# Performance work log

Measured on AMD Instinct MI355X. Metric: run time of the kernel, lower is better.

## Reference

```python
import jax, jax.numpy as jnp
import numpy as np

B, L, D, H = 2, 2048, 1024, 16
P = D // H  # head dim = 64


def setup_inputs() -> dict:
    key = jax.random.key(0)
    ks = jax.random.split(key, 9)
    s = 1.0 / np.sqrt(D)
    x = jax.random.normal(ks[0], (B, L, D), dtype=jnp.float32)
    Wq = jax.random.normal(ks[1], (D, D), dtype=jnp.float32) * s
    bq = jax.random.normal(ks[2], (D,), dtype=jnp.float32) * 0.02
    Wk = jax.random.normal(ks[3], (D, D), dtype=jnp.float32) * s
    bk = jax.random.normal(ks[4], (D,), dtype=jnp.float32) * 0.02
    Wv = jax.random.normal(ks[5], (D, D), dtype=jnp.float32) * s
    bv = jax.random.normal(ks[6], (D,), dtype=jnp.float32) * 0.02
    Wo = jax.random.normal(ks[7], (D, D), dtype=jnp.float32) * s
    bo = jax.random.normal(ks[8], (D,), dtype=jnp.float32) * 0.02
    return {"token_activations": x, "Wq": Wq, "bq": bq, "Wk": Wk, "bk": bk,
            "Wv": Wv, "bv": bv, "Wo": Wo, "bo": bo}


def _split_heads(t):
    # 'b l (h p) -> b h l p'
    b, l, d = t.shape
    return t.reshape(b, l, H, P).transpose(0, 2, 1, 3)


def reference(token_activations, Wq, bq, Wk, bk, Wv, bv, Wo, bo):
    x = token_activations
    q = _split_heads(x @ Wq.T + bq)  # [B,H,L,P]
    k = _split_heads(x @ Wk.T + bk)
    v = _split_heads(x @ Wv.T + bv)
    # pattern[b,h,l,m] = K_l . Q_m / sqrt(P)
    scores = jnp.einsum('bhlp,bhmp->bhlm', k, q) / jnp.sqrt(jnp.float32(P))
    attn = jax.nn.softmax(scores, axis=-2)  # softmax over key axis l
    # out at query position m: sum_l attn[l,m] * V_l
    o = jnp.einsum('bhlm,bhlp->bhmp', attn, v)  # [B,H,L,P] (m indexed)
    o = o.transpose(0, 2, 1, 3).reshape(x.shape[0], x.shape[1], D)  # 'b h m p -> b m (h p)'
    return o @ Wo.T + bo
```

## Files before the change

kernel.cpp:

```cpp
#include <hip/hip_runtime.h>

typedef unsigned short u16;
typedef float f32x4 __attribute__((ext_vector_type(4)));
typedef __bf16 bf16x8 __attribute__((ext_vector_type(8)));
typedef __bf16 bf16x4 __attribute__((ext_vector_type(4)));

#define DEV static __device__ __forceinline__

constexpr int kB = 2;
constexpr int kL = 2048;
constexpr int kD = 1024;
constexpr int kH = 16;
constexpr int kP = 64;
constexpr int kM = kB * kL;
constexpr float kQScale = 0.125f * 1.44269504088896f;

DEV u16 f2bf(float x) {
  union { float f; unsigned u; } v;
  v.f = x;
  unsigned r = v.u + 0x7fffu + ((v.u >> 16) & 1u);
  return (u16)(r >> 16);
}

DEV void gload16(const void* g, void* l) {
  __builtin_amdgcn_global_load_lds(
      (const __attribute__((address_space(1))) unsigned int*)g,
      (__attribute__((address_space(3))) unsigned int*)l, 16, 0, 0);
}

__global__ void cvt_kernel(const float* __restrict__ src, u16* __restrict__ dst, int n4) {
  int i = blockIdx.x * blockDim.x + threadIdx.x;
  if (i >= n4) return;
  float4 v = reinterpret_cast<const float4*>(src)[i];
  uint2 o;
  o.x = (unsigned)f2bf(v.x) | ((unsigned)f2bf(v.y) << 16);
  o.y = (unsigned)f2bf(v.z) | ((unsigned)f2bf(v.w) << 16);
  reinterpret_cast<uint2*>(dst)[i] = o;
}

__global__ void cvtw_kernel(const float* __restrict__ w0, const float* __restrict__ w1,
                            const float* __restrict__ w2, const float* __restrict__ w3,
                            u16* __restrict__ o0, u16* __restrict__ o1,
                            u16* __restrict__ o2, u16* __restrict__ o3) {
  int sel = blockIdx.x >> 10;
  int i = (blockIdx.x & 1023) * 256 + threadIdx.x;
  const float* src = sel == 0 ? w0 : (sel == 1 ? w1 : (sel == 2 ? w2 : w3));
  u16* dst = sel == 0 ? o0 : (sel == 1 ? o1 : (sel == 2 ? o2 : o3));
  float4 v = reinterpret_cast<const float4*>(src)[i];
  uint2 o;
  o.x = (unsigned)f2bf(v.x) | ((unsigned)f2bf(v.y) << 16);
  o.y = (unsigned)f2bf(v.z) | ((unsigned)f2bf(v.w) << 16);
  reinterpret_cast<uint2*>(dst)[i] = o;
}

template <bool SWAP>
DEV void gemm_tile(const u16* __restrict__ A, const u16* __restrict__ W,
                   int m0, int n0, u16* As, u16* Bs, f32x4 acc[4][4]) {
  const int tid = threadIdx.x;
  const int w = tid >> 6, lane = tid & 63;
  const int wr = w >> 1, wc = w & 1;
  const int g = lane >> 4, c = lane & 15;
  const int srow = lane >> 2;
  const int skoff = ((lane & 3) ^ (srow & 3)) * 8;
  const int rsl0 = (g ^ (c & 3)) * 8;

  for (int k0 = 0; k0 < kD; k0 += 32) {
    __syncthreads();
#pragma unroll
    for (int j = 0; j < 2; ++j) {
      const u16* ga = A + (size_t)(m0 + w * 32 + j * 16 + srow) * kD + k0 + skoff;
      gload16(ga, As + (w * 32 + j * 16) * 32);
      const u16* gb = W + (size_t)(n0 + w * 32 + j * 16 + srow) * kD + k0 + skoff;
      gload16(gb, Bs + (w * 32 + j * 16) * 32);
    }
    __syncthreads();

    bf16x8 af[4], bfr[4];
#pragma unroll
    for (int f = 0; f < 4; ++f) {
      af[f]  = *reinterpret_cast<const bf16x8*>(As + (wr * 64 + f * 16 + c) * 32 + rsl0);
      bfr[f] = *reinterpret_cast<const bf16x8*>(Bs + (wc * 64 + f * 16 + c) * 32 + rsl0);
    }
#pragma unroll
    for (int fi = 0; fi < 4; ++fi)
#pragma unroll
      for (int fj = 0; fj < 4; ++fj) {
        if constexpr (SWAP)
          acc[fj][fi] = __builtin_amdgcn_mfma_f32_16x16x32_bf16(bfr[fj], af[fi], acc[fj][fi], 0, 0, 0);
        else
          acc[fi][fj] = __builtin_amdgcn_mfma_f32_16x16x32_bf16(af[fi], bfr[fj], acc[fi][fj], 0, 0, 0);
      }
  }
}

__global__ __launch_bounds__(256) void qkv_kernel(
    const u16* __restrict__ xb,
    const u16* __restrict__ wq, const u16* __restrict__ wk, const u16* __restrict__ wv,
    const float* __restrict__ bq, const float* __restrict__ bk, const float* __restrict__ bv,
    u16* __restrict__ qb, u16* __restrict__ kb, u16* __restrict__ vtb) {
  __shared__ u16 As[128 * 32], Bs[128 * 32];
  const int mb = blockIdx.x, nb = blockIdx.y;
  const int sel = nb >> 3;
  const int m0 = mb * 128, n0 = (nb & 7) * 128;
  const u16* W = sel == 0 ? wq : (sel == 1 ? wk : wv);
  const float* bias = sel == 0 ? bq : (sel == 1 ? bk : bv);

  const int lane = threadIdx.x & 63, w = threadIdx.x >> 6;
  const int wr = w >> 1, wc = w & 1, g = lane >> 4, c = lane & 15;
  const int bb = m0 >> 11;
  const int lbase = (m0 & 2047) + wr * 64;

  f32x4 acc[4][4];
#pragma unroll
  for (int i = 0; i < 4; ++i)
#pragma unroll
    for (int j = 0; j < 4; ++j) acc[i][j] = f32x4{0.f, 0.f, 0.f, 0.f};

  if (sel < 2) {
    gemm_tile<true>(xb, W, m0, n0, As, Bs, acc);
    u16* dst = sel == 0 ? qb : kb;
    const float scale = (sel == 0) ? kQScale : 1.0f;
#pragma unroll
    for (int fj = 0; fj < 4; ++fj) {
      const int n4 = n0 + wc * 64 + fj * 16 + g * 4;
      const float4 b4 = *reinterpret_cast<const float4*>(&bias[n4]);
      const int hh = n4 >> 6, p0 = n4 & 63;
      u16* base = dst + ((size_t)(bb * kH + hh)) * kL * kP + p0;
#pragma unroll
      for (int fi = 0; fi < 4; ++fi) {
        const int l = lbase + fi * 16 + c;
        bf16x4 o;
        o[0] = (__bf16)((acc[fj][fi][0] + b4.x) * scale);
        o[1] = (__bf16)((acc[fj][fi][1] + b4.y) * scale);
        o[2] = (__bf16)((acc[fj][fi][2] + b4.z) * scale);
        o[3] = (__bf16)((acc[fj][fi][3] + b4.w) * scale);
        *reinterpret_cast<bf16x4*>(base + (size_t)l * kP) = o;
      }
    }
  } else {
    gemm_tile<false>(xb, W, m0, n0, As, Bs, acc);
#pragma unroll
    for (int fj = 0; fj < 4; ++fj) {
      const int n = n0 + wc * 64 + fj * 16 + c;
      const float bv_ = bias[n];
      const int hh = n >> 6, p = n & 63;
      u16* base = vtb + (((size_t)(bb * kH + hh)) * kP + p) * kL;
#pragma unroll
      for (int fi = 0; fi < 4; ++fi) {
        const int l4 = lbase + fi * 16 + g * 4;
        bf16x4 o;
#pragma unroll
        for (int r = 0; r < 4; ++r) o[r] = (__bf16)(acc[fi][fj][r] + bv_);
        *reinterpret_cast<bf16x4*>(base + l4) = o;
      }
    }
  }
}

__global__ __launch_bounds__(256) void out_kernel(
    const u16* __restrict__ ob, const u16* __restrict__ wo,
    const float* __restrict__ bo, float* __restrict__ out) {
  __shared__ u16 As[128 * 32], Bs[128 * 32];
  const int m0 = blockIdx.x * 128, n0 = blockIdx.y * 128;
  f32x4 acc[4][4];
#pragma unroll
  for (int i = 0; i < 4; ++i)
#pragma unroll
    for (int j = 0; j < 4; ++j) acc[i][j] = f32x4{0.f, 0.f, 0.f, 0.f};

  gemm_tile<true>(ob, wo, m0, n0, As, Bs, acc);

  const int lane = threadIdx.x & 63, w = threadIdx.x >> 6;
  const int wr = w >> 1, wc = w & 1, g = lane >> 4, c = lane & 15;
#pragma unroll
  for (int fj = 0; fj < 4; ++fj) {
    const int n4 = n0 + wc * 64 + fj * 16 + g * 4;
    const float4 b4 = *reinterpret_cast<const float4*>(&bo[n4]);
#pragma unroll
    for (int fi = 0; fi < 4; ++fi) {
      const int m = m0 + wr * 64 + fi * 16 + c;
      float4 o;
      o.x = acc[fj][fi][0] + b4.x;
      o.y = acc[fj][fi][1] + b4.y;
      o.z = acc[fj][fi][2] + b4.z;
      o.w = acc[fj][fi][3] + b4.w;
      *reinterpret_cast<float4*>(&out[(size_t)m * kD + n4]) = o;
    }
  }
}

__global__ __launch_bounds__(512, 2) void attn_kernel(
    const u16* __restrict__ qb, const u16* __restrict__ kb,
    const u16* __restrict__ vtb, u16* __restrict__ ob) {
  __shared__ __align__(16) char kvs[2][2][8192];
  __shared__ __align__(16) char pts[8][2048];
  const int tid = threadIdx.x, w = tid >> 6, lane = tid & 63;
  const int g = lane >> 4, c = lane & 15;
  const int h = blockIdx.y, b = blockIdx.z;
  const size_t hoff = ((size_t)(b * kH + h)) * kL * kP;
  const char* Qg = (const char*)(qb + hoff);
  const char* Kg = (const char*)(kb + hoff);
  const char* Vg = (const char*)(vtb + hoff);
  const int q0 = blockIdx.x * 128 + w * 16;

  const int lrow = lane >> 3;
  const int spb = ((lane & 7) ^ lrow) << 4;
  const char* kp = Kg + (size_t)(w * 8 + lrow) * 128 + spb;
  const char* vp = Vg + (size_t)(w * 8 + lrow) * (kL * 2) + spb;

  auto stage = [&](int buf) {
    gload16(kp, &kvs[buf][0][w * 1024]);
    gload16(vp, &kvs[buf][1][w * 1024]);
    kp += 64 * 128;
    vp += 128;
  };

  const int csw = (c & 7) << 4;
  const int kvb0 = c * 128 + ((g * 16) ^ csw);
  const int kvb1 = c * 128 + ((64 + g * 16) ^ csw);
  char* myPt = &pts[w][0];

  bf16x8 qf[2];
#pragma unroll
  for (int kc = 0; kc < 2; ++kc)
    qf[kc] = *reinterpret_cast<const bf16x8*>(Qg + (size_t)(q0 + c) * 128 + kc * 64 + g * 16);

  f32x4 oacc[4];
#pragma unroll
  for (int pt = 0; pt < 4; ++pt) oacc[pt] = f32x4{0.f, 0.f, 0.f, 0.f};
  float Srun = 0.f;

  stage(0);
  __syncthreads();

  constexpr int NT = kL / 64;
  auto body = [&](int cur, int t) {
    if (t + 1 < NT) stage(cur ^ 1);
    const char* Ks = &kvs[cur][0][0];
    const char* Vs = &kvs[cur][1][0];

    f32x4 s[4];
    __builtin_amdgcn_s_setprio(1);
#pragma unroll
    for (int lt = 0; lt < 4; ++lt) {
      bf16x8 k0 = *reinterpret_cast<const bf16x8*>(Ks + lt * 2048 + kvb0);
      bf16x8 k1 = *reinterpret_cast<const bf16x8*>(Ks + lt * 2048 + kvb1);
      f32x4 z = f32x4{0.f, 0.f, 0.f, 0.f};
      z = __builtin_amdgcn_mfma_f32_16x16x32_bf16(k0, qf[0], z, 0, 0, 0);
      z = __builtin_amdgcn_mfma_f32_16x16x32_bf16(k1, qf[1], z, 0, 0, 0);
      s[lt] = z;
    }
    __builtin_amdgcn_s_setprio(0);

    float tsum = 0.f;
#pragma unroll
    for (int lt = 0; lt < 4; ++lt) {
      bf16x4 pv;
#pragma unroll
      for (int r = 0; r < 4; ++r) {
        float p = __builtin_amdgcn_exp2f(s[lt][r]);
        tsum += p;
        pv[r] = (__bf16)p;
      }
      *reinterpret_cast<bf16x4*>(myPt + c * 128 + ((lt * 32 + g * 8) ^ csw)) = pv;
    }
    Srun += tsum;

    bf16x8 pf0 = *reinterpret_cast<const bf16x8*>(myPt + kvb0);
    bf16x8 pf1 = *reinterpret_cast<const bf16x8*>(myPt + kvb1);
    __builtin_amdgcn_s_setprio(1);
#pragma unroll
    for (int pt = 0; pt < 4; ++pt) {
      bf16x8 v0 = *reinterpret_cast<const bf16x8*>(Vs + pt * 2048 + kvb0);
      bf16x8 v1 = *reinterpret_cast<const bf16x8*>(Vs + pt * 2048 + kvb1);
      oacc[pt] = __builtin_amdgcn_mfma_f32_16x16x32_bf16(pf0, v0, oacc[pt], 0, 0, 0);
      oacc[pt] = __builtin_amdgcn_mfma_f32_16x16x32_bf16(pf1, v1, oacc[pt], 0, 0, 0);
    }
    __builtin_amdgcn_s_setprio(0);
    __syncthreads();
  };

  for (int t = 0; t < NT; t += 2) {
    body(0, t);
    body(1, t + 1);
  }

  Srun += __shfl_xor(Srun, 16, 64);
  Srun += __shfl_xor(Srun, 32, 64);

  float rs = 1.f / Srun;
  float fr[4];
#pragma unroll
  for (int r = 0; r < 4; ++r) fr[r] = __shfl(rs, g * 4 + r, 64);
#pragma unroll
  for (int pt = 0; pt < 4; ++pt)
#pragma unroll
    for (int r = 0; r < 4; ++r) {
      int q = q0 + g * 4 + r;
      ob[((size_t)(b * kL + q)) * kD + h * kP + pt * 16 + c] = f2bf(oacc[pt][r] * fr[r]);
    }
}

extern "C" void kernel_launch(void* const* d_in, const int* in_sizes, int n_in,
                              void* d_out, int out_size, void* d_ws, size_t ws_size,
                              hipStream_t stream) {
  (void)in_sizes; (void)n_in; (void)out_size; (void)ws_size;
  const float* x  = (const float*)d_in[0];
  const float* Wq = (const float*)d_in[1];
  const float* bq = (const float*)d_in[2];
  const float* Wk = (const float*)d_in[3];
  const float* bk = (const float*)d_in[4];
  const float* Wv = (const float*)d_in[5];
  const float* bv = (const float*)d_in[6];
  const float* Wo = (const float*)d_in[7];
  const float* bo = (const float*)d_in[8];
  float* out = (float*)d_out;

  char* ws = (char*)d_ws;
  u16* xb  = (u16*)(ws);
  u16* wqb = (u16*)(ws + (8u << 20));
  u16* wkb = (u16*)(ws + (10u << 20));
  u16* wvb = (u16*)(ws + (12u << 20));
  u16* wob = (u16*)(ws + (14u << 20));
  u16* qb  = (u16*)(ws + (16u << 20));
  u16* kb  = (u16*)(ws + (24u << 20));
  u16* vtb = (u16*)(ws + (32u << 20));

  cvt_kernel<<<kM * kD / 1024, 256, 0, stream>>>(x, xb, kM * kD / 4);
  cvtw_kernel<<<4096, 256, 0, stream>>>(Wq, Wk, Wv, Wo, wqb, wkb, wvb, wob);

  qkv_kernel<<<dim3(kM / 128, 24), 256, 0, stream>>>(
      xb, wqb, wkb, wvb, bq, bk, bv, qb, kb, vtb);

  attn_kernel<<<dim3(kL / 128, kH, kB), 512, 0, stream>>>(qb, kb, vtb, xb);

  out_kernel<<<dim3(kM / 128, kD / 128), 256, 0, stream>>>(xb, wob, bo, out);
}
```

Before: 117.6 us.

## Merge conversion kernels, remap GEMM blocks across XCDs, widen output GEMM to 512 threads

Combines the activation and weight bf16 conversion kernels into one launch to save a kernel launch. Remaps QKV and output GEMM block indices so that consecutive hardware blocks spread across the 8 XCDs, which is meant to improve L2 locality. Rewrites the output projection to use 8 waves per 128x128 tile with a smaller per-wave accumulator, giving more waves to hide latency. In exchange, each output wave issues more LDS reads per MFMA.

Result: no change. 116.2 us (-1.2%).

```diff
diff --git a/kernel.cpp b/kernel.cpp
--- a/kernel.cpp
+++ b/kernel.cpp
@@ -28,29 +28,29 @@
       (__attribute__((address_space(3))) unsigned int*)l, 16, 0, 0);
 }
 
-__global__ void cvt_kernel(const float* __restrict__ src, u16* __restrict__ dst, int n4) {
+__global__ void cvt_all(const float* __restrict__ x,
+                        const float* __restrict__ w0, const float* __restrict__ w1,
+                        const float* __restrict__ w2, const float* __restrict__ w3,
+                        u16* __restrict__ xb,
+                        u16* __restrict__ o0, u16* __restrict__ o1,
+                        u16* __restrict__ o2, u16* __restrict__ o3) {
   int i = blockIdx.x * blockDim.x + threadIdx.x;
-  if (i >= n4) return;
-  float4 v = reinterpret_cast<const float4*>(src)[i];
+  const float* src;
+  u16* dst;
+  int j;
+  if (i < (1 << 20)) {
+    src = x; dst = xb; j = i;
+  } else {
+    int s = (i >> 18) & 3;
+    j = i & ((1 << 18) - 1);
+    src = s == 0 ? w0 : (s == 1 ? w1 : (s == 2 ? w2 : w3));
+    dst = s == 0 ? o0 : (s == 1 ? o1 : (s == 2 ? o2 : o3));
+  }
+  float4 v = reinterpret_cast<const float4*>(src)[j];
   uint2 o;
   o.x = (unsigned)f2bf(v.x) | ((unsigned)f2bf(v.y) << 16);
   o.y = (unsigned)f2bf(v.z) | ((unsigned)f2bf(v.w) << 16);
-  reinterpret_cast<uint2*>(dst)[i] = o;
-}
-
-__global__ void cvtw_kernel(const float* __restrict__ w0, const float* __restrict__ w1,
-                            const float* __restrict__ w2, const float* __restrict__ w3,
-                            u16* __restrict__ o0, u16* __restrict__ o1,
-                            u16* __restrict__ o2, u16* __restrict__ o3) {
-  int sel = blockIdx.x >> 10;
-  int i = (blockIdx.x & 1023) * 256 + threadIdx.x;
-  const float* src = sel == 0 ? w0 : (sel == 1 ? w1 : (sel == 2 ? w2 : w3));
-  u16* dst = sel == 0 ? o0 : (sel == 1 ? o1 : (sel == 2 ? o2 : o3));
-  float4 v = reinterpret_cast<const float4*>(src)[i];
-  uint2 o;
-  o.x = (unsigned)f2bf(v.x) | ((unsigned)f2bf(v.y) << 16);
-  o.y = (unsigned)f2bf(v.z) | ((unsigned)f2bf(v.w) << 16);
-  reinterpret_cast<uint2*>(dst)[i] = o;
+  reinterpret_cast<uint2*>(dst)[j] = o;
 }
 
 template <bool SWAP>
@@ -99,7 +99,9 @@
     const float* __restrict__ bq, const float* __restrict__ bk, const float* __restrict__ bv,
     u16* __restrict__ qb, u16* __restrict__ kb, u16* __restrict__ vtb) {
   __shared__ u16 As[128 * 32], Bs[128 * 32];
-  const int mb = blockIdx.x, nb = blockIdx.y;
+  const int hw = blockIdx.x;
+  const int logical = (hw & 7) * 96 + (hw >> 3);
+  const int mb = logical & 31, nb = logical >> 5;
   const int sel = nb >> 3;
   const int m0 = mb * 128, n0 = (nb & 7) * 128;
   const u16* W = sel == 0 ? wq : (sel == 1 ? wk : wv);
@@ -157,24 +159,55 @@
   }
 }
 
-__global__ __launch_bounds__(256) void out_kernel(
+__global__ __launch_bounds__(512) void out_kernel(
     const u16* __restrict__ ob, const u16* __restrict__ wo,
     const float* __restrict__ bo, float* __restrict__ out) {
   __shared__ u16 As[128 * 32], Bs[128 * 32];
-  const int m0 = blockIdx.x * 128, n0 = blockIdx.y * 128;
-  f32x4 acc[4][4];
-#pragma unroll
-  for (int i = 0; i < 4; ++i)
+  const int hw = blockIdx.x;
+  const int logical = (hw & 7) * 32 + (hw >> 3);
+  const int m0 = (logical & 31) * 128, n0 = (logical >> 5) * 128;
+
+  const int tid = threadIdx.x;
+  const int w = tid >> 6, lane = tid & 63;
+  const int wr = w >> 2, wc = w & 3;
+  const int g = lane >> 4, c = lane & 15;
+  const int srow = lane >> 2;
+  const int skoff = ((lane & 3) ^ (srow & 3)) * 8;
+  const int rsl0 = (g ^ (c & 3)) * 8;
+
+  f32x4 acc[2][4];
+#pragma unroll
+  for (int i = 0; i < 2; ++i)
 #pragma unroll
     for (int j = 0; j < 4; ++j) acc[i][j] = f32x4{0.f, 0.f, 0.f, 0.f};
 
-  gemm_tile<true>(ob, wo, m0, n0, As, Bs, acc);
-
-  const int lane = threadIdx.x & 63, w = threadIdx.x >> 6;
-  const int wr = w >> 1, wc = w & 1, g = lane >> 4, c = lane & 15;
-#pragma unroll
-  for (int fj = 0; fj < 4; ++fj) {
-    const int n4 = n0 + wc * 64 + fj * 16 + g * 4;
+  for (int k0 = 0; k0 < kD; k0 += 32) {
+    __syncthreads();
+    {
+      const u16* ga = ob + (size_t)(m0 + w * 16 + srow) * kD + k0 + skoff;
+      gload16(ga, As + (w * 16) * 32);
+      const u16* gb = wo + (size_t)(n0 + w * 16 + srow) * kD + k0 + skoff;
+      gload16(gb, Bs + (w * 16) * 32);
+    }
+    __syncthreads();
+
+    bf16x8 af[4], bfr[2];
+#pragma unroll
+    for (int f = 0; f < 4; ++f)
+      af[f] = *reinterpret_cast<const bf16x8*>(As + (wr * 64 + f * 16 + c) * 32 + rsl0);
+#pragma unroll
+    for (int f = 0; f < 2; ++f)
+      bfr[f] = *reinterpret_cast<const bf16x8*>(Bs + (wc * 32 + f * 16 + c) * 32 + rsl0);
+#pragma unroll
+    for (int fj = 0; fj < 2; ++fj)
+#pragma unroll
+      for (int fi = 0; fi < 4; ++fi)
+        acc[fj][fi] = __builtin_amdgcn_mfma_f32_16x16x32_bf16(bfr[fj], af[fi], acc[fj][fi], 0, 0, 0);
+  }
+
+#pragma unroll
+  for (int fj = 0; fj < 2; ++fj) {
+    const int n4 = n0 + wc * 32 + fj * 16 + g * 4;
     const float4 b4 = *reinterpret_cast<const float4*>(&bo[n4]);
 #pragma unroll
     for (int fi = 0; fi < 4; ++fi) {
@@ -326,13 +359,12 @@
   u16* kb  = (u16*)(ws + (24u << 20));
   u16* vtb = (u16*)(ws + (32u << 20));
 
-  cvt_kernel<<<kM * kD / 1024, 256, 0, stream>>>(x, xb, kM * kD / 4);
-  cvtw_kernel<<<4096, 256, 0, stream>>>(Wq, Wk, Wv, Wo, wqb, wkb, wvb, wob);
-
-  qkv_kernel<<<dim3(kM / 128, 24), 256, 0, stream>>>(
+  cvt_all<<<8192, 256, 0, stream>>>(x, Wq, Wk, Wv, Wo, xb, wqb, wkb, wvb, wob);
+
+  qkv_kernel<<<768, 256, 0, stream>>>(
       xb, wqb, wkb, wvb, bq, bk, bv, qb, kb, vtb);
 
   attn_kernel<<<dim3(kL / 128, kH, kB), 512, 0, stream>>>(qb, kb, vtb, xb);
 
-  out_kernel<<<dim3(kM / 128, kD / 128), 256, 0, stream>>>(xb, wob, bo, out);
-}
+  out_kernel<<<256, 512, 0, stream>>>(xb, wob, bo, out);
+}
```
